# Kernel tuning notes

Measured on AMD Instinct MI355X. Metric: run time of the kernel, lower is better.

## Reference

```python
import jax, jax.numpy as jnp
import numpy as np

N = 20000      # n_nodes
L = 4          # lamb_len (number of decay rates)
M = 64         # memory_dimension (= message_dimension)
F = 128        # node feature dim
E = 128        # embedding_dimension
B = 100000     # number of interaction events in the batch
RAW = 2 * M * L + F + 1  # 641, raw message dim
H = RAW // 2   # MLP hidden dim


def setup_inputs() -> dict:
    key = jax.random.key(0)
    ks = jax.random.split(key, 18)
    s = lambda d: 1.0 / np.sqrt(d)
    inp = {
        "node_features": jax.random.normal(ks[0], (N, F), jnp.float32),
        "memory": jax.random.normal(ks[1], (N, L, M), jnp.float32) * 0.1,
        "last_update": jnp.zeros((N,), jnp.float32),
        "lambs": jnp.array([1.0, 0.1, 0.01, 0.001], jnp.float32),
        "theta": jnp.array([0.5], jnp.float32),
        "static_emb": jax.random.normal(ks[2], (N, E), jnp.float32),
        "W1": jax.random.normal(ks[3], (H, RAW), jnp.float32) * s(RAW),
        "b1": jnp.zeros((H,), jnp.float32),
        "W2": jax.random.normal(ks[4], (M, H), jnp.float32) * s(H),
        "b2": jnp.zeros((M,), jnp.float32),
        "We": jax.random.normal(ks[5], (M, L * M), jnp.float32) * s(L * M),
        "be": jnp.zeros((M,), jnp.float32),
        "Ws": jax.random.normal(ks[6], (E, M), jnp.float32) * s(M),
        "bs": jnp.zeros((E,), jnp.float32),
        "timestamps": jax.random.uniform(ks[7], (B,), jnp.float32) * 1000.0,
        "source_nodes": jax.random.randint(ks[8], (B,), 0, N),
        "target_nodes": jax.random.randint(ks[9], (B,), 0, N),
    }
    return inp


def reference(node_features, memory, last_update, lambs, theta, static_emb,
              W1, b1, W2, b2, We, be, Ws, bs,
              timestamps, source_nodes, target_nodes):
    n, l, m = memory.shape
    b = source_nodes.shape[0]
    mem_flat = memory.reshape(n, l * m)

    # ---- temporal memory gather + raw message build: [B, RAW] ----
    src_emb = mem_flat[source_nodes]
    tgt_emb = mem_flat[target_nodes]
    raw = jnp.concatenate(
        [src_emb, tgt_emb, node_features[target_nodes],
         jnp.ones((b, 1), memory.dtype)], axis=1)

    # ---- exp_lambs aggregation per source node ----
    t_node = jax.ops.segment_max(timestamps, source_nodes, num_segments=n)
    counts = jax.ops.segment_sum(jnp.ones_like(timestamps), source_nodes,
                                 num_segments=n)
    has = counts > 0
    t_node_safe = jnp.where(has, t_node, last_update)  # latest event time per node
    dt = t_node_safe[source_nodes] - timestamps        # [B], >= 0
    w = jnp.exp(-dt[:, None] * lambs[None, :])         # [B, L] decay weights
    # decayed sum of raw messages per node, per lambda: [N, L, RAW]
    agg = jnp.stack(
        [jax.ops.segment_sum(w[:, li:li + 1] * raw, source_nodes,
                             num_segments=n) for li in range(l)], axis=1)

    # ---- MLP message function: [N, L, M] ----
    h = jax.nn.relu(jnp.einsum('nlr,hr->nlh', agg, W1) + b1)
    msg = jnp.einsum('nlh,mh->nlm', h, W2) + b2

    # ---- exp memory update ----
    decay = jnp.exp(-(t_node_safe - last_update)[:, None] * lambs[None, :])  # [N, L]
    updated = memory * decay[..., None] + jnp.where(has[:, None, None], msg, 0.0)

    # ---- embedding fusion ----
    dyn = updated.reshape(n, l * m)
    e = jax.nn.leaky_relu(dyn @ We.T + be, negative_slope=0.01)
    s = jax.nn.leaky_relu(e @ Ws.T + bs, negative_slope=0.01)
    embeddings = theta * static_emb + (1.0 - theta) * s
    return embeddings
```

## Files before the change

kernel.cpp:

```cpp
#include <hip/hip_runtime.h>

constexpr int LDIM = 4;
constexpr int MDIM = 64;
constexpr int FDIM = 128;
constexpr int EDIM = 128;
constexpr int RAWD = 641;
constexpr int HDIM = 320;
constexpr int LM   = LDIM * MDIM;
constexpr int KXY  = LM + FDIM;
constexpr int NXY  = 2 * HDIM;

typedef short bf16x8 __attribute__((ext_vector_type(8)));
typedef short bf16x4 __attribute__((ext_vector_type(4)));
typedef float f32x4  __attribute__((ext_vector_type(4)));

__device__ __forceinline__ void split_bf16(float x, unsigned short& h, unsigned short& l)
{
    unsigned xb = __float_as_uint(x);
    unsigned short hh = (unsigned short)(xb >> 16);
    float hf = __uint_as_float(((unsigned)hh) << 16);
    float r  = x - hf;
    h = hh;
    l = (unsigned short)(__float_as_uint(r) >> 16);
}

__global__ void k_init(int* t_node_bits, int* counts, int* cursor2, int* cursor, int Nn)
{
    int n = blockIdx.x * blockDim.x + threadIdx.x;
    if (n < Nn) {
        t_node_bits[n] = 0xBF800000;
        counts[n]  = 0;
        cursor2[n] = 0;
    }
    if (n == 0) cursor[0] = 0;
}

__global__ void k_ev1(const int* __restrict__ src, const float* __restrict__ ts,
                      int* t_node_bits, int* counts, int Bev)
{
    int b = blockIdx.x * blockDim.x + threadIdx.x;
    if (b >= Bev) return;
    int s = src[b];
    atomicMax(&t_node_bits[s], __float_as_int(ts[b]));
    atomicAdd(&counts[s], 1);
}

__global__ void k_node(const int* __restrict__ t_node_bits, const int* __restrict__ counts,
                       const float* __restrict__ last_update, const float* __restrict__ lambs,
                       float* t_safe, float* decay, int* start, int* cursor, int Nn)
{
    int n = blockIdx.x * blockDim.x + threadIdx.x;
    if (n >= Nn) return;
    int c = counts[n];
    float lu = last_update[n];
    float tsn = (c > 0) ? __int_as_float(t_node_bits[n]) : lu;
    t_safe[n] = tsn;
    float d = tsn - lu;
    #pragma unroll
    for (int li = 0; li < LDIM; ++li)
        decay[n * LDIM + li] = expf(-d * lambs[li]);
    start[n] = atomicAdd(cursor, c);
}

__global__ void k_ev2(const int* __restrict__ src, const int* __restrict__ tgt,
                      const float* __restrict__ ts, const float* __restrict__ t_safe,
                      const int* __restrict__ start, int* cursor2,
                      const float* __restrict__ lambs,
                      int* sorted_tgt, float4* sorted_w, int Bev)
{
    int b = blockIdx.x * blockDim.x + threadIdx.x;
    if (b >= Bev) return;
    int s = src[b];
    int pos = start[s] + atomicAdd(&cursor2[s], 1);
    sorted_tgt[pos] = tgt[b];
    float dt = t_safe[s] - ts[b];
    sorted_w[pos] = make_float4(expf(-dt * lambs[0]), expf(-dt * lambs[1]),
                                expf(-dt * lambs[2]), expf(-dt * lambs[3]));
}

__global__ void k_prep(const float* __restrict__ W1, const float* __restrict__ W2,
                       const float* __restrict__ We, const float* __restrict__ Ws,
                       unsigned short* WpTh, unsigned short* WpTl,
                       unsigned short* W2h,  unsigned short* W2l,
                       unsigned short* Weh,  unsigned short* Wel,
                       unsigned short* Wsh,  unsigned short* Wsl)
{
    int idx = blockIdx.x * blockDim.x + threadIdx.x;
    constexpr int T1 = NXY * KXY;
    constexpr int T2 = MDIM * HDIM;
    constexpr int T3 = MDIM * LM;
    constexpr int T4 = EDIM * MDIM;
    unsigned short h, l;
    if (idx < T1) {
        int n = idx / KXY, k = idx % KXY;
        float v;
        if (n < HDIM) {
            v = (k < LM) ? W1[(long)n * RAWD + k] : 0.f;
        } else {
            int hh = n - HDIM;
            v = (k < LM) ? W1[(long)hh * RAWD + LM + k]
                         : W1[(long)hh * RAWD + 2 * LM + (k - LM)];
        }
        split_bf16(v, h, l); WpTh[idx] = h; WpTl[idx] = l;
    } else if (idx < T1 + T2) {
        int r = idx - T1;
        split_bf16(W2[r], h, l); W2h[r] = h; W2l[r] = l;
    } else if (idx < T1 + T2 + T3) {
        int r = idx - T1 - T2;
        split_bf16(We[r], h, l); Weh[r] = h; Wel[r] = l;
    } else if (idx < T1 + T2 + T3 + T4) {
        int r = idx - T1 - T2 - T3;
        split_bf16(Ws[r], h, l); Wsh[r] = h; Wsl[r] = l;
    }
}

__global__ __launch_bounds__(HDIM) void k_gather(
    const float* __restrict__ C1, const float4* __restrict__ sorted_w,
    const int* __restrict__ sorted_tgt, const int* __restrict__ start,
    const int* __restrict__ counts,
    const float* __restrict__ W1, const float* __restrict__ b1,
    unsigned short* __restrict__ hh, unsigned short* __restrict__ hl, int Nn)
{
    const int tid = threadIdx.x;
    const float bb = b1[tid];
    const float w1last = W1[(long)tid * RAWD + (RAWD - 1)];
    for (int n = blockIdx.x; n < Nn; n += gridDim.x) {
        int cnt = counts[n];
        if (cnt == 0) continue;
        int st = start[n];
        float z0 = 0, z1 = 0, z2 = 0, z3 = 0;
        float s0 = 0, s1 = 0, s2 = 0, s3 = 0;
        for (int e = 0; e < cnt; ++e) {
            float4 w = sorted_w[st + e];
            int    t = sorted_tgt[st + e];
            float yv = C1[(long)t * NXY + HDIM + tid];
            z0 += w.x * yv; z1 += w.y * yv; z2 += w.z * yv; z3 += w.w * yv;
            s0 += w.x;      s1 += w.y;      s2 += w.z;      s3 += w.w;
        }
        float xv = C1[(long)n * NXY + tid] + w1last;
        long base = ((long)n * LDIM) * HDIM + tid;
        unsigned short a, b_;
        float h0 = fmaxf(xv * s0 + z0 + bb, 0.f);
        split_bf16(h0, a, b_); hh[base] = a; hl[base] = b_;
        float h1 = fmaxf(xv * s1 + z1 + bb, 0.f);
        split_bf16(h1, a, b_); hh[base + HDIM] = a; hl[base + HDIM] = b_;
        float h2 = fmaxf(xv * s2 + z2 + bb, 0.f);
        split_bf16(h2, a, b_); hh[base + 2 * HDIM] = a; hl[base + 2 * HDIM] = b_;
        float h3 = fmaxf(xv * s3 + z3 + bb, 0.f);
        split_bf16(h3, a, b_); hh[base + 3 * HDIM] = a; hl[base + 3 * HDIM] = b_;
    }
}

template <int BN, int AF32, int EPI>
__global__ __launch_bounds__(256) void k_mgemm(
    const float* __restrict__ A0, const float* __restrict__ A1,
    int lda0, int lda1, int ksplit,
    const unsigned short* __restrict__ Agh, const unsigned short* __restrict__ Agl,
    const unsigned short* __restrict__ Bgh, const unsigned short* __restrict__ Bgl,
    float* __restrict__ Cf, unsigned short* __restrict__ Coh, unsigned short* __restrict__ Col,
    int M, int N, int K,
    const float* __restrict__ bias, const float* __restrict__ x1,
    const float* __restrict__ x2, const int* __restrict__ icnts,
    const float* __restrict__ theta)
{
    constexpr int BM = 128, BK = 32;
    constexpr int SN = BN / 32;
    __shared__ unsigned short Ash[BM * BK], Asl[BM * BK];
    __shared__ unsigned short Bsh[BN * BK], Bsl[BN * BK];
    const int tid  = threadIdx.x;
    const int w    = tid >> 6, lane = tid & 63;
    const int wm   = w >> 1,   wn   = w & 1;
    const int lrow = lane & 15, lq = lane >> 4;
    const long m0 = (long)blockIdx.x * BM;
    const int  n0 = blockIdx.y * BN;

    f32x4 acc[4][SN];
    #pragma unroll
    for (int s = 0; s < 4; ++s)
        #pragma unroll
        for (int t = 0; t < SN; ++t) acc[s][t] = (f32x4){0.f, 0.f, 0.f, 0.f};

    for (int k0 = 0; k0 < K; k0 += BK) {
        if constexpr (AF32) {
            #pragma unroll
            for (int it = 0; it < 4; ++it) {
                int c = it * 256 + tid;
                int row = c >> 3, kc = c & 7;
                long gm = m0 + row; if (gm > M - 1) gm = M - 1;
                int gk = k0 + kc * 4;
                const float* sp = (gk < ksplit) ? (A0 + gm * (long)lda0 + gk)
                                                : (A1 + gm * (long)lda1 + (gk - ksplit));
                float4 v = *(const float4*)sp;
                unsigned short h0,l0,h1,l1,h2,l2,h3,l3;
                split_bf16(v.x, h0, l0); split_bf16(v.y, h1, l1);
                split_bf16(v.z, h2, l2); split_bf16(v.w, h3, l3);
                int soff = row * BK + (((kc >> 1) ^ (row & 3)) << 3) + (kc & 1) * 4;
                *(bf16x4*)&Ash[soff] = (bf16x4){(short)h0,(short)h1,(short)h2,(short)h3};
                *(bf16x4*)&Asl[soff] = (bf16x4){(short)l0,(short)l1,(short)l2,(short)l3};
            }
        } else {
            #pragma unroll
            for (int it = 0; it < 2; ++it) {
                int c = it * 256 + tid;
                int row = c >> 2, kc = c & 3;
                long gm = m0 + row; if (gm > M - 1) gm = M - 1;
                long goff = gm * (long)K + k0 + kc * 8;
                int soff = row * BK + ((kc ^ (row & 3)) << 3);
                *(int4*)&Ash[soff] = *(const int4*)(Agh + goff);
                *(int4*)&Asl[soff] = *(const int4*)(Agl + goff);
            }
        }
        #pragma unroll
        for (int it = 0; it < BN / 64; ++it) {
            int c = it * 256 + tid;
            int row = c >> 2, kc = c & 3;
            long goff = (long)(n0 + row) * K + k0 + kc * 8;
            int soff = row * BK + ((kc ^ (row & 3)) << 3);
            *(int4*)&Bsh[soff] = *(const int4*)(Bgh + goff);
            *(int4*)&Bsl[soff] = *(const int4*)(Bgl + goff);
        }
        __syncthreads();

        bf16x8 ah[4], al[4], bh[SN], bl[SN];
        #pragma unroll
        for (int s = 0; s < 4; ++s) {
            int row = wm * 64 + s * 16 + lrow;
            int off = row * BK + ((lq ^ (row & 3)) << 3);
            ah[s] = *(const bf16x8*)&Ash[off];
            al[s] = *(const bf16x8*)&Asl[off];
        }
        #pragma unroll
        for (int t = 0; t < SN; ++t) {
            int row = wn * (BN / 2) + t * 16 + lrow;
            int off = row * BK + ((lq ^ (row & 3)) << 3);
            bh[t] = *(const bf16x8*)&Bsh[off];
            bl[t] = *(const bf16x8*)&Bsl[off];
        }
        #pragma unroll
        for (int s = 0; s < 4; ++s)
            #pragma unroll
            for (int t = 0; t < SN; ++t) {
                acc[s][t] = __builtin_amdgcn_mfma_f32_16x16x32_bf16(ah[s], bh[t], acc[s][t], 0, 0, 0);
                acc[s][t] = __builtin_amdgcn_mfma_f32_16x16x32_bf16(ah[s], bl[t], acc[s][t], 0, 0, 0);
                acc[s][t] = __builtin_amdgcn_mfma_f32_16x16x32_bf16(al[s], bh[t], acc[s][t], 0, 0, 0);
            }
        __syncthreads();
    }

    float th = 0.f;
    if constexpr (EPI == 3) th = theta[0];
    #pragma unroll
    for (int s = 0; s < 4; ++s) {
        #pragma unroll
        for (int t = 0; t < SN; ++t) {
            #pragma unroll
            for (int r = 0; r < 4; ++r) {
                long grow = m0 + wm * 64 + s * 16 + lq * 4 + r;
                if (grow >= M) continue;
                int col = n0 + wn * (BN / 2) + t * 16 + lrow;
                float v = acc[s][t][r];
                long idx = grow * (long)N + col;
                if constexpr (EPI == 0) {
                    Cf[idx] = v;
                } else if constexpr (EPI == 1) {
                    float vb = v + bias[col];
                    bool has = icnts[grow >> 2] > 0;
                    float u = x1[idx] * x2[grow] + (has ? vb : 0.f);
                    unsigned short hq, lq2; split_bf16(u, hq, lq2);
                    Coh[idx] = hq; Col[idx] = lq2;
                } else if constexpr (EPI == 2) {
                    float u = v + bias[col];
                    u = u > 0.f ? u : 0.01f * u;
                    unsigned short hq, lq2; split_bf16(u, hq, lq2);
                    Coh[idx] = hq; Col[idx] = lq2;
                } else {
                    float u = v + bias[col];
                    u = u > 0.f ? u : 0.01f * u;
                    Cf[idx] = th * x1[idx] + (1.f - th) * u;
                }
            }
        }
    }
}

extern "C" void kernel_launch(void* const* d_in, const int* in_sizes, int n_in,
                              void* d_out, int out_size, void* d_ws, size_t ws_size,
                              hipStream_t stream)
{
    (void)n_in; (void)out_size; (void)ws_size;
    const float* node_features = (const float*)d_in[0];
    const float* memory        = (const float*)d_in[1];
    const float* last_update   = (const float*)d_in[2];
    const float* lambs         = (const float*)d_in[3];
    const float* theta         = (const float*)d_in[4];
    const float* static_emb    = (const float*)d_in[5];
    const float* W1            = (const float*)d_in[6];
    const float* b1            = (const float*)d_in[7];
    const float* W2            = (const float*)d_in[8];
    const float* b2            = (const float*)d_in[9];
    const float* We            = (const float*)d_in[10];
    const float* be            = (const float*)d_in[11];
    const float* Ws            = (const float*)d_in[12];
    const float* bs            = (const float*)d_in[13];
    const float* timestamps    = (const float*)d_in[14];
    const int*   src           = (const int*)d_in[15];
    const int*   tgt           = (const int*)d_in[16];
    float* out = (float*)d_out;

    const int Nn  = in_sizes[2];
    const int Bev = in_sizes[14];

    char* base = (char*)d_ws;
    size_t off = 0;
    auto take = [&](size_t bytes) -> void* {
        off = (off + 255) & ~(size_t)255;
        void* r = base + off;
        off += bytes;
        return r;
    };
    int*   t_node_bits = (int*)  take((size_t)Nn * 4);
    int*   counts      = (int*)  take((size_t)Nn * 4);
    int*   startb      = (int*)  take((size_t)Nn * 4);
    int*   cursor2     = (int*)  take((size_t)Nn * 4);
    int*   cursor      = (int*)  take(256);
    float* t_safe      = (float*)take((size_t)Nn * 4);
    float* decay       = (float*)take((size_t)Nn * LDIM * 4);
    int*   sorted_tgt  = (int*)  take((size_t)Bev * 4);
    float4* sorted_w   = (float4*)take((size_t)Bev * 16);
    unsigned short* WpTh = (unsigned short*)take((size_t)NXY * KXY * 2);
    unsigned short* WpTl = (unsigned short*)take((size_t)NXY * KXY * 2);
    unsigned short* W2h  = (unsigned short*)take((size_t)MDIM * HDIM * 2);
    unsigned short* W2l  = (unsigned short*)take((size_t)MDIM * HDIM * 2);
    unsigned short* Weh  = (unsigned short*)take((size_t)MDIM * LM * 2);
    unsigned short* Wel  = (unsigned short*)take((size_t)MDIM * LM * 2);
    unsigned short* Wsh  = (unsigned short*)take((size_t)EDIM * MDIM * 2);
    unsigned short* Wsl  = (unsigned short*)take((size_t)EDIM * MDIM * 2);
    float*          C1   = (float*)take((size_t)Nn * NXY * 4);
    unsigned short* hh   = (unsigned short*)take((size_t)Nn * LDIM * HDIM * 2);
    unsigned short* hl   = (unsigned short*)take((size_t)Nn * LDIM * HDIM * 2);
    unsigned short* updh = (unsigned short*)take((size_t)Nn * LM * 2);
    unsigned short* updl = (unsigned short*)take((size_t)Nn * LM * 2);
    unsigned short* eh   = (unsigned short*)take((size_t)Nn * MDIM * 2);
    unsigned short* el   = (unsigned short*)take((size_t)Nn * MDIM * 2);

    const int tb = 256;
    k_init<<<(Nn + tb - 1) / tb, tb, 0, stream>>>(t_node_bits, counts, cursor2, cursor, Nn);
    k_ev1<<<(Bev + tb - 1) / tb, tb, 0, stream>>>(src, timestamps, t_node_bits, counts, Bev);
    k_node<<<(Nn + tb - 1) / tb, tb, 0, stream>>>(t_node_bits, counts, last_update, lambs,
                                                  t_safe, decay, startb, cursor, Nn);
    k_ev2<<<(Bev + tb - 1) / tb, tb, 0, stream>>>(src, tgt, timestamps, t_safe,
                                                  startb, cursor2, lambs,
                                                  sorted_tgt, sorted_w, Bev);
    const int preptot = NXY * KXY + MDIM * HDIM + MDIM * LM + EDIM * MDIM;
    k_prep<<<(preptot + tb - 1) / tb, tb, 0, stream>>>(W1, W2, We, Ws,
                                                       WpTh, WpTl, W2h, W2l,
                                                       Weh, Wel, Wsh, Wsl);

    const int mb1 = (Nn + 127) / 128;

    k_mgemm<128, 1, 0><<<dim3(mb1, NXY / 128), 256, 0, stream>>>(
        memory, node_features, LM, FDIM, LM,
        nullptr, nullptr, WpTh, WpTl,
        C1, nullptr, nullptr, Nn, NXY, KXY,
        nullptr, nullptr, nullptr, nullptr, nullptr);

    k_gather<<<2048, HDIM, 0, stream>>>(C1, sorted_w, sorted_tgt, startb, counts,
                                        W1, b1, hh, hl, Nn);

    k_mgemm<64, 0, 1><<<dim3(Nn * LDIM / 128, 1), 256, 0, stream>>>(
        nullptr, nullptr, 0, 0, 0,
        hh, hl, W2h, W2l,
        nullptr, updh, updl, Nn * LDIM, MDIM, HDIM,
        b2, memory, decay, counts, nullptr);

    k_mgemm<64, 0, 2><<<dim3(mb1, 1), 256, 0, stream>>>(
        nullptr, nullptr, 0, 0, 0,
        updh, updl, Weh, Wel,
        nullptr, eh, el, Nn, MDIM, LM,
        be, nullptr, nullptr, nullptr, nullptr);

    k_mgemm<128, 0, 3><<<dim3(mb1, 1), 256, 0, stream>>>(
        nullptr, nullptr, 0, 0, 0,
        eh, el, Wsh, Wsl,
        out, nullptr, nullptr, Nn, EDIM, MDIM,
        bs, static_emb, nullptr, nullptr, theta);
}
```

Before: 321.4 us.

## Switch split-bf16 GEMMs to fp16 activations with two-term scaled fp16 weights

Replaces the three-MFMA split-bf16 emulation of fp32 GEMMs with a two-MFMA scheme: activations are stored as single fp16, and weights are split into scaled hi/lo fp16 pairs. Intermediate buffers (C1, h, updated memory, e) become single fp16 arrays, which halves their traffic and removes the lo-part loads. A separate kernel pre-packs memory and node features to fp16. The gather kernel now assigns one wavefront per node instead of one block per node. This lowers precision of activations to fp16, which risks accuracy loss or overflow.

```diff
diff --git a/kernel.cpp b/kernel.cpp
--- a/kernel.cpp
+++ b/kernel.cpp
@@ -10,19 +10,11 @@
 constexpr int KXY  = LM + FDIM;
 constexpr int NXY  = 2 * HDIM;
 
-typedef short bf16x8 __attribute__((ext_vector_type(8)));
-typedef short bf16x4 __attribute__((ext_vector_type(4)));
-typedef float f32x4  __attribute__((ext_vector_type(4)));
-
-__device__ __forceinline__ void split_bf16(float x, unsigned short& h, unsigned short& l)
-{
-    unsigned xb = __float_as_uint(x);
-    unsigned short hh = (unsigned short)(xb >> 16);
-    float hf = __uint_as_float(((unsigned)hh) << 16);
-    float r  = x - hf;
-    h = hh;
-    l = (unsigned short)(__float_as_uint(r) >> 16);
-}
+typedef _Float16 f16x8 __attribute__((ext_vector_type(8)));
+typedef float    f32x4 __attribute__((ext_vector_type(4)));
+
+constexpr float WSCALE  = 256.f;
+constexpr float WSINV   = 1.f / 256.f;
 
 __global__ void k_init(int* t_node_bits, int* counts, int* cursor2, int* cursor, int Nn)
 {
@@ -78,22 +70,29 @@
                                 expf(-dt * lambs[2]), expf(-dt * lambs[3]));
 }
 
+__global__ void k_half(const float* __restrict__ mem, const float* __restrict__ nf,
+                       _Float16* __restrict__ A1, int total)
+{
+    int idx = blockIdx.x * blockDim.x + threadIdx.x;
+    if (idx >= total) return;
+    int n = idx / KXY, k = idx % KXY;
+    float v = (k < LM) ? mem[(long)n * LM + k] : nf[(long)n * FDIM + (k - LM)];
+    A1[idx] = (_Float16)v;
+}
+
 __global__ void k_prep(const float* __restrict__ W1, const float* __restrict__ W2,
                        const float* __restrict__ We, const float* __restrict__ Ws,
-                       unsigned short* WpTh, unsigned short* WpTl,
-                       unsigned short* W2h,  unsigned short* W2l,
-                       unsigned short* Weh,  unsigned short* Wel,
-                       unsigned short* Wsh,  unsigned short* Wsl)
+                       _Float16* WpH, _Float16* WpL, _Float16* W2H, _Float16* W2L,
+                       _Float16* WeH, _Float16* WeL, _Float16* WsH, _Float16* WsL)
 {
     int idx = blockIdx.x * blockDim.x + threadIdx.x;
     constexpr int T1 = NXY * KXY;
     constexpr int T2 = MDIM * HDIM;
     constexpr int T3 = MDIM * LM;
     constexpr int T4 = EDIM * MDIM;
-    unsigned short h, l;
+    float v; _Float16 *H, *L; int o;
     if (idx < T1) {
         int n = idx / KXY, k = idx % KXY;
-        float v;
         if (n < HDIM) {
             v = (k < LM) ? W1[(long)n * RAWD + k] : 0.f;
         } else {
@@ -101,63 +100,75 @@
             v = (k < LM) ? W1[(long)hh * RAWD + LM + k]
                          : W1[(long)hh * RAWD + 2 * LM + (k - LM)];
         }
-        split_bf16(v, h, l); WpTh[idx] = h; WpTl[idx] = l;
+        H = WpH; L = WpL; o = idx;
     } else if (idx < T1 + T2) {
-        int r = idx - T1;
-        split_bf16(W2[r], h, l); W2h[r] = h; W2l[r] = l;
+        o = idx - T1; v = W2[o]; H = W2H; L = W2L;
     } else if (idx < T1 + T2 + T3) {
-        int r = idx - T1 - T2;
-        split_bf16(We[r], h, l); Weh[r] = h; Wel[r] = l;
+        o = idx - T1 - T2; v = We[o]; H = WeH; L = WeL;
     } else if (idx < T1 + T2 + T3 + T4) {
-        int r = idx - T1 - T2 - T3;
-        split_bf16(Ws[r], h, l); Wsh[r] = h; Wsl[r] = l;
-    }
-}
-
-__global__ __launch_bounds__(HDIM) void k_gather(
-    const float* __restrict__ C1, const float4* __restrict__ sorted_w,
-    const int* __restrict__ sorted_tgt, const int* __restrict__ start,
+        o = idx - T1 - T2 - T3; v = Ws[o]; H = WsH; L = WsL;
+    } else return;
+    float xs = WSCALE * v;
+    _Float16 hh = (_Float16)xs;
+    _Float16 ll = (_Float16)(xs - (float)hh);
+    H[o] = hh; L[o] = ll;
+}
+
+__global__ __launch_bounds__(256) void k_gather(
+    const _Float16* __restrict__ C1, const float4* __restrict__ sorted_w,
+    const int* __restrict__ sorted_tgt, const int* __restrict__ startb,
     const int* __restrict__ counts,
     const float* __restrict__ W1, const float* __restrict__ b1,
-    unsigned short* __restrict__ hh, unsigned short* __restrict__ hl, int Nn)
-{
-    const int tid = threadIdx.x;
-    const float bb = b1[tid];
-    const float w1last = W1[(long)tid * RAWD + (RAWD - 1)];
-    for (int n = blockIdx.x; n < Nn; n += gridDim.x) {
+    _Float16* __restrict__ h, int Nn)
+{
+    const int lane = threadIdx.x & 63;
+    const int wv   = threadIdx.x >> 6;
+    float bb[5], wl[5];
+    #pragma unroll
+    for (int c = 0; c < 5; ++c) {
+        int hi = c * 64 + lane;
+        bb[c] = b1[hi];
+        wl[c] = W1[(long)hi * RAWD + (RAWD - 1)];
+    }
+    for (int n = blockIdx.x * 4 + wv; n < Nn; n += gridDim.x * 4) {
         int cnt = counts[n];
         if (cnt == 0) continue;
-        int st = start[n];
-        float z0 = 0, z1 = 0, z2 = 0, z3 = 0;
-        float s0 = 0, s1 = 0, s2 = 0, s3 = 0;
+        int st = startb[n];
+        float z[5][4];
+        float sw[4] = {0.f, 0.f, 0.f, 0.f};
+        #pragma unroll
+        for (int c = 0; c < 5; ++c)
+            #pragma unroll
+            for (int li = 0; li < 4; ++li) z[c][li] = 0.f;
         for (int e = 0; e < cnt; ++e) {
             float4 w = sorted_w[st + e];
             int    t = sorted_tgt[st + e];
-            float yv = C1[(long)t * NXY + HDIM + tid];
-            z0 += w.x * yv; z1 += w.y * yv; z2 += w.z * yv; z3 += w.w * yv;
-            s0 += w.x;      s1 += w.y;      s2 += w.z;      s3 += w.w;
-        }
-        float xv = C1[(long)n * NXY + tid] + w1last;
-        long base = ((long)n * LDIM) * HDIM + tid;
-        unsigned short a, b_;
-        float h0 = fmaxf(xv * s0 + z0 + bb, 0.f);
-        split_bf16(h0, a, b_); hh[base] = a; hl[base] = b_;
-        float h1 = fmaxf(xv * s1 + z1 + bb, 0.f);
-        split_bf16(h1, a, b_); hh[base + HDIM] = a; hl[base + HDIM] = b_;
-        float h2 = fmaxf(xv * s2 + z2 + bb, 0.f);
-        split_bf16(h2, a, b_); hh[base + 2 * HDIM] = a; hl[base + 2 * HDIM] = b_;
-        float h3 = fmaxf(xv * s3 + z3 + bb, 0.f);
-        split_bf16(h3, a, b_); hh[base + 3 * HDIM] = a; hl[base + 3 * HDIM] = b_;
-    }
-}
-
-template <int BN, int AF32, int EPI>
+            const _Float16* yr = C1 + (long)t * NXY + HDIM;
+            sw[0] += w.x; sw[1] += w.y; sw[2] += w.z; sw[3] += w.w;
+            #pragma unroll
+            for (int c = 0; c < 5; ++c) {
+                float yv = (float)yr[c * 64 + lane];
+                z[c][0] += w.x * yv; z[c][1] += w.y * yv;
+                z[c][2] += w.z * yv; z[c][3] += w.w * yv;
+            }
+        }
+        #pragma unroll
+        for (int c = 0; c < 5; ++c) {
+            float xv = (float)C1[(long)n * NXY + c * 64 + lane] + wl[c];
+            #pragma unroll
+            for (int li = 0; li < 4; ++li) {
+                float hv = xv * sw[li] + z[c][li] + bb[c];
+                h[((long)n * LDIM + li) * HDIM + c * 64 + lane] = (_Float16)fmaxf(hv, 0.f);
+            }
+        }
+    }
+}
+
+template <int BN, int EPI>
 __global__ __launch_bounds__(256) void k_mgemm(
-    const float* __restrict__ A0, const float* __restrict__ A1,
-    int lda0, int lda1, int ksplit,
-    const unsigned short* __restrict__ Agh, const unsigned short* __restrict__ Agl,
-    const unsigned short* __restrict__ Bgh, const unsigned short* __restrict__ Bgl,
-    float* __restrict__ Cf, unsigned short* __restrict__ Coh, unsigned short* __restrict__ Col,
+    const _Float16* __restrict__ Ag,
+    const _Float16* __restrict__ Bgh, const _Float16* __restrict__ Bgl,
+    _Float16* __restrict__ Ch, float* __restrict__ Cf,
     int M, int N, int K,
     const float* __restrict__ bias, const float* __restrict__ x1,
     const float* __restrict__ x2, const int* __restrict__ icnts,
@@ -165,8 +176,8 @@
 {
     constexpr int BM = 128, BK = 32;
     constexpr int SN = BN / 32;
-    __shared__ unsigned short Ash[BM * BK], Asl[BM * BK];
-    __shared__ unsigned short Bsh[BN * BK], Bsl[BN * BK];
+    __shared__ _Float16 Ash[BM * BK];
+    __shared__ _Float16 Bsh[BN * BK], Bsl[BN * BK];
     const int tid  = threadIdx.x;
     const int w    = tid >> 6, lane = tid & 63;
     const int wm   = w >> 1,   wn   = w & 1;
@@ -181,34 +192,14 @@
         for (int t = 0; t < SN; ++t) acc[s][t] = (f32x4){0.f, 0.f, 0.f, 0.f};
 
     for (int k0 = 0; k0 < K; k0 += BK) {
-        if constexpr (AF32) {
-            #pragma unroll
-            for (int it = 0; it < 4; ++it) {
-                int c = it * 256 + tid;
-                int row = c >> 3, kc = c & 7;
-                long gm = m0 + row; if (gm > M - 1) gm = M - 1;
-                int gk = k0 + kc * 4;
-                const float* sp = (gk < ksplit) ? (A0 + gm * (long)lda0 + gk)
-                                                : (A1 + gm * (long)lda1 + (gk - ksplit));
-                float4 v = *(const float4*)sp;
-                unsigned short h0,l0,h1,l1,h2,l2,h3,l3;
-                split_bf16(v.x, h0, l0); split_bf16(v.y, h1, l1);
-                split_bf16(v.z, h2, l2); split_bf16(v.w, h3, l3);
-                int soff = row * BK + (((kc >> 1) ^ (row & 3)) << 3) + (kc & 1) * 4;
-                *(bf16x4*)&Ash[soff] = (bf16x4){(short)h0,(short)h1,(short)h2,(short)h3};
-                *(bf16x4*)&Asl[soff] = (bf16x4){(short)l0,(short)l1,(short)l2,(short)l3};
-            }
-        } else {
-            #pragma unroll
-            for (int it = 0; it < 2; ++it) {
-                int c = it * 256 + tid;
-                int row = c >> 2, kc = c & 3;
-                long gm = m0 + row; if (gm > M - 1) gm = M - 1;
-                long goff = gm * (long)K + k0 + kc * 8;
-                int soff = row * BK + ((kc ^ (row & 3)) << 3);
-                *(int4*)&Ash[soff] = *(const int4*)(Agh + goff);
-                *(int4*)&Asl[soff] = *(const int4*)(Agl + goff);
-            }
+        #pragma unroll
+        for (int it = 0; it < 2; ++it) {
+            int c = it * 256 + tid;
+            int row = c >> 2, kc = c & 3;
+            long gm = m0 + row; if (gm > M - 1) gm = M - 1;
+            long goff = gm * (long)K + k0 + kc * 8;
+            int soff = row * BK + ((kc ^ (row & 3)) << 3);
+            *(int4*)&Ash[soff] = *(const int4*)(Ag + goff);
         }
         #pragma unroll
         for (int it = 0; it < BN / 64; ++it) {
@@ -221,28 +212,26 @@
         }
         __syncthreads();
 
-        bf16x8 ah[4], al[4], bh[SN], bl[SN];
+        f16x8 a[4], bh[SN], bl[SN];
         #pragma unroll
         for (int s = 0; s < 4; ++s) {
             int row = wm * 64 + s * 16 + lrow;
             int off = row * BK + ((lq ^ (row & 3)) << 3);
-            ah[s] = *(const bf16x8*)&Ash[off];
-            al[s] = *(const bf16x8*)&Asl[off];
+            a[s] = *(const f16x8*)&Ash[off];
         }
         #pragma unroll
         for (int t = 0; t < SN; ++t) {
             int row = wn * (BN / 2) + t * 16 + lrow;
             int off = row * BK + ((lq ^ (row & 3)) << 3);
-            bh[t] = *(const bf16x8*)&Bsh[off];
-            bl[t] = *(const bf16x8*)&Bsl[off];
+            bh[t] = *(const f16x8*)&Bsh[off];
+            bl[t] = *(const f16x8*)&Bsl[off];
         }
         #pragma unroll
         for (int s = 0; s < 4; ++s)
             #pragma unroll
             for (int t = 0; t < SN; ++t) {
-                acc[s][t] = __builtin_amdgcn_mfma_f32_16x16x32_bf16(ah[s], bh[t], acc[s][t], 0, 0, 0);
-                acc[s][t] = __builtin_amdgcn_mfma_f32_16x16x32_bf16(ah[s], bl[t], acc[s][t], 0, 0, 0);
-                acc[s][t] = __builtin_amdgcn_mfma_f32_16x16x32_bf16(al[s], bh[t], acc[s][t], 0, 0, 0);
+                acc[s][t] = __builtin_amdgcn_mfma_f32_16x16x32_f16(a[s], bh[t], acc[s][t], 0, 0, 0);
+                acc[s][t] = __builtin_amdgcn_mfma_f32_16x16x32_f16(a[s], bl[t], acc[s][t], 0, 0, 0);
             }
         __syncthreads();
     }
@@ -258,21 +247,19 @@
                 long grow = m0 + wm * 64 + s * 16 + lq * 4 + r;
                 if (grow >= M) continue;
                 int col = n0 + wn * (BN / 2) + t * 16 + lrow;
-                float v = acc[s][t][r];
+                float v = acc[s][t][r] * WSINV;
                 long idx = grow * (long)N + col;
                 if constexpr (EPI == 0) {
-                    Cf[idx] = v;
+                    Ch[idx] = (_Float16)v;
                 } else if constexpr (EPI == 1) {
                     float vb = v + bias[col];
                     bool has = icnts[grow >> 2] > 0;
                     float u = x1[idx] * x2[grow] + (has ? vb : 0.f);
-                    unsigned short hq, lq2; split_bf16(u, hq, lq2);
-                    Coh[idx] = hq; Col[idx] = lq2;
+                    Ch[idx] = (_Float16)u;
                 } else if constexpr (EPI == 2) {
                     float u = v + bias[col];
                     u = u > 0.f ? u : 0.01f * u;
-                    unsigned short hq, lq2; split_bf16(u, hq, lq2);
-                    Coh[idx] = hq; Col[idx] = lq2;
+                    Ch[idx] = (_Float16)u;
                 } else {
                     float u = v + bias[col];
                     u = u > 0.f ? u : 0.01f * u;
@@ -318,30 +305,28 @@
         off += bytes;
         return r;
     };
-    int*   t_node_bits = (int*)  take((size_t)Nn * 4);
-    int*   counts      = (int*)  take((size_t)Nn * 4);
-    int*   startb      = (int*)  take((size_t)Nn * 4);
-    int*   cursor2     = (int*)  take((size_t)Nn * 4);
-    int*   cursor      = (int*)  take(256);
-    float* t_safe      = (float*)take((size_t)Nn * 4);
-    float* decay       = (float*)take((size_t)Nn * LDIM * 4);
-    int*   sorted_tgt  = (int*)  take((size_t)Bev * 4);
-    float4* sorted_w   = (float4*)take((size_t)Bev * 16);
-    unsigned short* WpTh = (unsigned short*)take((size_t)NXY * KXY * 2);
-    unsigned short* WpTl = (unsigned short*)take((size_t)NXY * KXY * 2);
-    unsigned short* W2h  = (unsigned short*)take((size_t)MDIM * HDIM * 2);
-    unsigned short* W2l  = (unsigned short*)take((size_t)MDIM * HDIM * 2);
-    unsigned short* Weh  = (unsigned short*)take((size_t)MDIM * LM * 2);
-    unsigned short* Wel  = (unsigned short*)take((size_t)MDIM * LM * 2);
-    unsigned short* Wsh  = (unsigned short*)take((size_t)EDIM * MDIM * 2);
-    unsigned short* Wsl  = (unsigned short*)take((size_t)EDIM * MDIM * 2);
-    float*          C1   = (float*)take((size_t)Nn * NXY * 4);
-    unsigned short* hh   = (unsigned short*)take((size_t)Nn * LDIM * HDIM * 2);
-    unsigned short* hl   = (unsigned short*)take((size_t)Nn * LDIM * HDIM * 2);
-    unsigned short* updh = (unsigned short*)take((size_t)Nn * LM * 2);
-    unsigned short* updl = (unsigned short*)take((size_t)Nn * LM * 2);
-    unsigned short* eh   = (unsigned short*)take((size_t)Nn * MDIM * 2);
-    unsigned short* el   = (unsigned short*)take((size_t)Nn * MDIM * 2);
+    int*    t_node_bits = (int*)   take((size_t)Nn * 4);
+    int*    counts      = (int*)   take((size_t)Nn * 4);
+    int*    startb      = (int*)   take((size_t)Nn * 4);
+    int*    cursor2     = (int*)   take((size_t)Nn * 4);
+    int*    cursor      = (int*)   take(256);
+    float*  t_safe      = (float*) take((size_t)Nn * 4);
+    float*  decay       = (float*) take((size_t)Nn * LDIM * 4);
+    int*    sorted_tgt  = (int*)   take((size_t)Bev * 4);
+    float4* sorted_w    = (float4*)take((size_t)Bev * 16);
+    _Float16* WpH = (_Float16*)take((size_t)NXY * KXY * 2);
+    _Float16* WpL = (_Float16*)take((size_t)NXY * KXY * 2);
+    _Float16* W2H = (_Float16*)take((size_t)MDIM * HDIM * 2);
+    _Float16* W2L = (_Float16*)take((size_t)MDIM * HDIM * 2);
+    _Float16* WeH = (_Float16*)take((size_t)MDIM * LM * 2);
+    _Float16* WeL = (_Float16*)take((size_t)MDIM * LM * 2);
+    _Float16* WsH = (_Float16*)take((size_t)EDIM * MDIM * 2);
+    _Float16* WsL = (_Float16*)take((size_t)EDIM * MDIM * 2);
+    _Float16* A1  = (_Float16*)take((size_t)Nn * KXY * 2);
+    _Float16* C1  = (_Float16*)take((size_t)Nn * NXY * 2);
+    _Float16* hbuf= (_Float16*)take((size_t)Nn * LDIM * HDIM * 2);
+    _Float16* updh= (_Float16*)take((size_t)Nn * LM * 2);
+    _Float16* ebuf= (_Float16*)take((size_t)Nn * MDIM * 2);
 
     const int tb = 256;
     k_init<<<(Nn + tb - 1) / tb, tb, 0, stream>>>(t_node_bits, counts, cursor2, cursor, Nn);
@@ -353,35 +338,29 @@
                                                   sorted_tgt, sorted_w, Bev);
     const int preptot = NXY * KXY + MDIM * HDIM + MDIM * LM + EDIM * MDIM;
     k_prep<<<(preptot + tb - 1) / tb, tb, 0, stream>>>(W1, W2, We, Ws,
-                                                       WpTh, WpTl, W2h, W2l,
-                                                       Weh, Wel, Wsh, Wsl);
+                                                       WpH, WpL, W2H, W2L,
+                                                       WeH, WeL, WsH, WsL);
+    const int packtot = Nn * KXY;
+    k_half<<<(packtot + tb - 1) / tb, tb, 0, stream>>>(memory, node_features, A1, packtot);
 
     const int mb1 = (Nn + 127) / 128;
 
-    k_mgemm<128, 1, 0><<<dim3(mb1, NXY / 128), 256, 0, stream>>>(
-        memory, node_features, LM, FDIM, LM,
-        nullptr, nullptr, WpTh, WpTl,
-        C1, nullptr, nullptr, Nn, NXY, KXY,
+    k_mgemm<128, 0><<<dim3(mb1, NXY / 128), 256, 0, stream>>>(
+        A1, WpH, WpL, C1, nullptr, Nn, NXY, KXY,
         nullptr, nullptr, nullptr, nullptr, nullptr);
 
-    k_gather<<<2048, HDIM, 0, stream>>>(C1, sorted_w, sorted_tgt, startb, counts,
-                                        W1, b1, hh, hl, Nn);
-
-    k_mgemm<64, 0, 1><<<dim3(Nn * LDIM / 128, 1), 256, 0, stream>>>(
-        nullptr, nullptr, 0, 0, 0,
-        hh, hl, W2h, W2l,
-        nullptr, updh, updl, Nn * LDIM, MDIM, HDIM,
+    k_gather<<<5000, 256, 0, stream>>>(C1, sorted_w, sorted_tgt, startb, counts,
+                                       W1, b1, hbuf, Nn);
+
+    k_mgemm<64, 1><<<dim3(Nn * LDIM / 128, 1), 256, 0, stream>>>(
+        hbuf, W2H, W2L, updh, nullptr, Nn * LDIM, MDIM, HDIM,
         b2, memory, decay, counts, nullptr);
 
-    k_mgemm<64, 0, 2><<<dim3(mb1, 1), 256, 0, stream>>>(
-        nullptr, nullptr, 0, 0, 0,
-        updh, updl, Weh, Wel,
-        nullptr, eh, el, Nn, MDIM, LM,
+    k_mgemm<64, 2><<<dim3(mb1, 1), 256, 0, stream>>>(
+        updh, WeH, WeL, ebuf, nullptr, Nn, MDIM, LM,
         be, nullptr, nullptr, nullptr, nullptr);
 
-    k_mgemm<128, 0, 3><<<dim3(mb1, 1), 256, 0, stream>>>(
-        nullptr, nullptr, 0, 0, 0,
-        eh, el, Wsh, Wsl,
-        out, nullptr, nullptr, Nn, EDIM, MDIM,
+    k_mgemm<128, 3><<<dim3(mb1, 1), 256, 0, stream>>>(
+        ebuf, WsH, WsL, nullptr, out, Nn, EDIM, MDIM,
         bs, static_emb, nullptr, nullptr, theta);
 }
```

New measurement: 299.4 us. 6.9% less time.
